# Kernel optimization log

Hardware: AMD Instinct MI355X
Metric: run time of the kernel (lower is better)

The kernel has to match this reference:

```python
import jax, jax.numpy as jnp
import numpy as np

B, T, IN, OUT = 32, 128, 512, 512
N, Wd, R, H = 128, 64, 4, 512      # memory slots, word size, read heads, controller size
EPS = 1e-6
IFACE = R * Wd + R + Wd + 1 + Wd + Wd + R + 1 + 1 + 3 * R  # DNC interface vector size


def setup_inputs() -> dict:
    key = jax.random.key(0)
    ks = jax.random.split(key, 6)
    s = jnp.float32(0.05)
    lstm_in = IN + R * Wd
    return {
        "input_sequence": jax.random.normal(ks[0], (B, T, IN), jnp.float32),
        "Wx": jax.random.normal(ks[1], (lstm_in, 4 * H), jnp.float32) * s,
        "Wh": jax.random.normal(ks[2], (H, 4 * H), jnp.float32) * s,
        "b_lstm": jnp.zeros((4 * H,), jnp.float32),
        "W_iface": jax.random.normal(ks[3], (H, IFACE), jnp.float32) * s,
        "b_iface": jnp.zeros((IFACE,), jnp.float32),
        "W_out": jax.random.normal(ks[4], (R * Wd + H, OUT), jnp.float32) * s,
        "b_out": jnp.zeros((OUT,), jnp.float32),
    }


def _alloc(u):
    """DNC allocation weighting for one example. u: [N] usage in [0,1]."""
    phi = jnp.argsort(u)                      # ascending usage (data-dependent gather)
    su = u[phi]
    cp = jnp.cumprod(su)
    cp_excl = jnp.concatenate([jnp.ones((1,), su.dtype), cp[:-1]])
    a_sorted = (1.0 - su) * cp_excl
    return jnp.zeros_like(u).at[phi].set(a_sorted)  # scatter back to original order


def _content(M, keys, beta):
    """Cosine content addressing. M: [B,N,W], keys: [B,K,W], beta: [B,K] -> [B,K,N]."""
    Mn = M / (jnp.linalg.norm(M, axis=-1, keepdims=True) + EPS)
    kn = keys / (jnp.linalg.norm(keys, axis=-1, keepdims=True) + EPS)
    sim = jnp.einsum('bnw,bkw->bkn', Mn, kn)
    return jax.nn.softmax(beta[..., None] * sim, axis=-1)


def _dnc_forward(input_sequence, Wx, Wh, b_lstm, W_iface, b_iface, W_out, b_out):
    eye = 1.0 - jnp.eye(N, dtype=jnp.float32)

    def step(carry, x_t):
        h, c, M, usage, link, prec, ww, wr, reads = carry
        # --- LSTM controller ---
        z = jnp.concatenate([x_t, reads], -1) @ Wx + h @ Wh + b_lstm
        i_g, f_g, g_g, o_g = jnp.split(z, 4, axis=-1)
        c_n = jax.nn.sigmoid(f_g) * c + jax.nn.sigmoid(i_g) * jnp.tanh(g_g)
        h_n = jax.nn.sigmoid(o_g) * jnp.tanh(c_n)
        # --- interface vector ---
        v = h_n @ W_iface + b_iface
        o = [0]
        def take(n):
            out = v[:, o[0]:o[0] + n]; o[0] += n; return out
        read_keys = take(R * Wd).reshape(B, R, Wd)
        read_beta = 1.0 + jax.nn.softplus(take(R))
        write_key = take(Wd).reshape(B, 1, Wd)
        write_beta = 1.0 + jax.nn.softplus(take(1))
        erase = jax.nn.sigmoid(take(Wd))
        write_vec = take(Wd)
        free = jax.nn.sigmoid(take(R))
        alloc_g = jax.nn.sigmoid(take(1))
        write_g = jax.nn.sigmoid(take(1))
        modes = jax.nn.softmax(take(3 * R).reshape(B, R, 3), axis=-1)
        # --- usage & allocation ---
        retention = jnp.prod(1.0 - free[:, :, None] * wr, axis=1)          # [B,N]
        usage_n = (usage + ww - usage * ww) * retention
        a = jax.vmap(_alloc)(usage_n)
        # --- write ---
        cw = _content(M, write_key, write_beta)[:, 0, :]                    # [B,N]
        ww_n = write_g * (alloc_g * a + (1.0 - alloc_g) * cw)
        M_n = M * (1.0 - ww_n[:, :, None] * erase[:, None, :]) + ww_n[:, :, None] * write_vec[:, None, :]
        # --- temporal link ---
        link_n = ((1.0 - ww_n[:, :, None] - ww_n[:, None, :]) * link
                  + ww_n[:, :, None] * prec[:, None, :]) * eye
        prec_n = (1.0 - ww_n.sum(-1, keepdims=True)) * prec + ww_n
        # --- read ---
        fw = jnp.einsum('bij,brj->bri', link_n, wr)
        bw = jnp.einsum('bji,brj->bri', link_n, wr)
        cr = _content(M_n, read_keys, read_beta)
        wr_n = modes[:, :, 0:1] * bw + modes[:, :, 1:2] * cr + modes[:, :, 2:3] * fw
        reads_n = jnp.einsum('brn,bnw->brw', wr_n, M_n).reshape(B, R * Wd)
        # --- output projection ---
        out = jnp.concatenate([reads_n, h_n], -1) @ W_out + b_out
        return (h_n, c_n, M_n, usage_n, link_n, prec_n, ww_n, wr_n, reads_n), out

    f32 = jnp.float32
    init = (jnp.zeros((B, H), f32), jnp.zeros((B, H), f32),
            jnp.zeros((B, N, Wd), f32), jnp.zeros((B, N), f32),
            jnp.zeros((B, N, N), f32), jnp.zeros((B, N), f32),
            jnp.zeros((B, N), f32), jnp.zeros((B, R, N), f32),
            jnp.zeros((B, R * Wd), f32))
    _, outs = jax.lax.scan(step, init, jnp.swapaxes(input_sequence, 0, 1))
    return jnp.swapaxes(outs, 0, 1)  # [B, T, OUT]


def reference(input_sequence, Wx, Wh, b_lstm, W_iface, b_iface, W_out, b_out):
    return _dnc_forward(input_sequence, Wx, Wh, b_lstm, W_iface, b_iface, W_out, b_out)
```

## Files before the change

### kernel.cpp

```cpp
#include <hip/hip_runtime.h>
#include <math.h>

#define TT 128
#define ZD 2048
#define IFC 471
#define EPSF 1e-6f
#define MST 66
#define LST 130
#define NBLK 256
#define UHT 24640
#define VHT 15424

#define FSP 16
#define NFLAGS 8192

#define D4(a,b) ((a).x*(b).x + (a).y*(b).y + (a).z*(b).z + (a).w*(b).w)

__device__ __forceinline__ float sig_(float x){ return 1.f/(1.f+expf(-x)); }
__device__ __forceinline__ float sp_(float x){ return fmaxf(x,0.f)+log1pf(expf(-fabsf(x))); }

__device__ __forceinline__ void st1(float* p, float v){
  unsigned u; __builtin_memcpy(&u,&v,4);
  __hip_atomic_store((unsigned*)p, u, __ATOMIC_RELAXED, __HIP_MEMORY_SCOPE_AGENT);
}
__device__ __forceinline__ void st2(float* p, float2 v){
  unsigned long long u; __builtin_memcpy(&u,&v,8);
  __hip_atomic_store((unsigned long long*)p, u, __ATOMIC_RELAXED, __HIP_MEMORY_SCOPE_AGENT);
}

__device__ __forceinline__ void arrive(unsigned* f, unsigned gen){
  __syncthreads();
  if (threadIdx.x == 0)
    __hip_atomic_store(f, gen, __ATOMIC_RELAXED, __HIP_MEMORY_SCOPE_AGENT);
}
__device__ __forceinline__ void wait_ge(const unsigned* f, int n, unsigned gen){
  if (threadIdx.x < 64){
    for (int i = threadIdx.x; i < n; i += 64){
      const unsigned* p = f + (size_t)i*FSP;
      if (__hip_atomic_load(p, __ATOMIC_RELAXED, __HIP_MEMORY_SCOPE_AGENT) >= gen) continue;
      int spins = 0; bool done = false;
      while (spins < 64){
        if (__hip_atomic_load(p, __ATOMIC_RELAXED, __HIP_MEMORY_SCOPE_AGENT) >= gen){ done = true; break; }
        __builtin_amdgcn_s_sleep(1); ++spins;
      }
      if (!done){
        while (__hip_atomic_load(p, __ATOMIC_RELAXED, __HIP_MEMORY_SCOPE_AGENT) < gen)
          __builtin_amdgcn_s_sleep(2);
      }
    }
  }
  __syncthreads();
}

__device__ __forceinline__ unsigned bf16rne(float f){
  unsigned u; __builtin_memcpy(&u,&f,4);
  return (u + 0x7fffu + ((u>>16)&1u)) >> 16;
}
__device__ __forceinline__ float bflo(unsigned w){
  unsigned u = w << 16; float f; __builtin_memcpy(&f,&u,4); return f;
}
__device__ __forceinline__ float bfhi(unsigned w){
  unsigned u = w & 0xffff0000u; float f; __builtin_memcpy(&f,&u,4); return f;
}

__global__ __launch_bounds__(256) void gemm_bias(
    const float* __restrict__ A, const float* __restrict__ B,
    const float* __restrict__ bias, float* __restrict__ C,
    int Nc, int K)
{
  __shared__ float As[16][68];
  __shared__ float Bs[16][68];
  const int tid = threadIdx.x;
  const int bx = blockIdx.x, by = blockIdx.y;
  const int tx = tid & 15, ty = tid >> 4;
  const int am = tid >> 2, ak = (tid & 3) * 4;
  const int bk = tid >> 4, bn = (tid & 15) * 4;
  float acc[4][4] = {};
  const float* Ap = A + (size_t)(by*64+am)*K + ak;
  const float* Bp = B + (size_t)bk*Nc + bx*64 + bn;
  for (int k0 = 0; k0 < K; k0 += 16) {
    float4 av = *(const float4*)Ap; Ap += 16;
    float4 bv = *(const float4*)Bp; Bp += (size_t)16*Nc;
    As[ak+0][am]=av.x; As[ak+1][am]=av.y; As[ak+2][am]=av.z; As[ak+3][am]=av.w;
    *(float4*)&Bs[bk][bn] = bv;
    __syncthreads();
#pragma unroll
    for (int kk = 0; kk < 16; ++kk) {
      float4 a4 = *(const float4*)&As[kk][ty*4];
      float4 b4 = *(const float4*)&Bs[kk][tx*4];
      acc[0][0]+=a4.x*b4.x; acc[0][1]+=a4.x*b4.y; acc[0][2]+=a4.x*b4.z; acc[0][3]+=a4.x*b4.w;
      acc[1][0]+=a4.y*b4.x; acc[1][1]+=a4.y*b4.y; acc[1][2]+=a4.y*b4.z; acc[1][3]+=a4.y*b4.w;
      acc[2][0]+=a4.z*b4.x; acc[2][1]+=a4.z*b4.y; acc[2][2]+=a4.z*b4.z; acc[2][3]+=a4.z*b4.w;
      acc[3][0]+=a4.w*b4.x; acc[3][1]+=a4.w*b4.y; acc[3][2]+=a4.w*b4.z; acc[3][3]+=a4.w*b4.w;
    }
    __syncthreads();
  }
  float4 bb = *(const float4*)(bias + bx*64 + tx*4);
#pragma unroll
  for (int i = 0; i < 4; ++i) {
    float4 o;
    o.x = acc[i][0]+bb.x; o.y = acc[i][1]+bb.y; o.z = acc[i][2]+bb.z; o.w = acc[i][3]+bb.w;
    *(float4*)(C + (size_t)(by*64+ty*4+i)*Nc + bx*64 + tx*4) = o;
  }
}

__global__ __launch_bounds__(256) void gemm_out(
    const float* __restrict__ A, const float* __restrict__ B,
    const float* __restrict__ bias, float* __restrict__ C)
{
  __shared__ float As[16][68];
  __shared__ float Bs[16][68];
  const int tid = threadIdx.x;
  const int bx = blockIdx.x, by = blockIdx.y;
  const int tx = tid & 15, ty = tid >> 4;
  const int am = tid >> 2, ak = (tid & 3) * 4;
  const int bk = tid >> 4, bn = (tid & 15) * 4;
  float acc[4][4] = {};
  const int arow = by*64 + am;
  const float* Ap = A + (size_t)(arow >> 5)*UHT + (size_t)(arow & 31)*768 + ak;
  const float* Bp = B + (size_t)bk*512 + bx*64 + bn;
  for (int k0 = 0; k0 < 768; k0 += 16) {
    float4 av = *(const float4*)Ap; Ap += 16;
    float4 bv = *(const float4*)Bp; Bp += (size_t)16*512;
    As[ak+0][am]=av.x; As[ak+1][am]=av.y; As[ak+2][am]=av.z; As[ak+3][am]=av.w;
    *(float4*)&Bs[bk][bn] = bv;
    __syncthreads();
#pragma unroll
    for (int kk = 0; kk < 16; ++kk) {
      float4 a4 = *(const float4*)&As[kk][ty*4];
      float4 b4 = *(const float4*)&Bs[kk][tx*4];
      acc[0][0]+=a4.x*b4.x; acc[0][1]+=a4.x*b4.y; acc[0][2]+=a4.x*b4.z; acc[0][3]+=a4.x*b4.w;
      acc[1][0]+=a4.y*b4.x; acc[1][1]+=a4.y*b4.y; acc[1][2]+=a4.y*b4.z; acc[1][3]+=a4.y*b4.w;
      acc[2][0]+=a4.z*b4.x; acc[2][1]+=a4.z*b4.y; acc[2][2]+=a4.z*b4.z; acc[2][3]+=a4.z*b4.w;
      acc[3][0]+=a4.w*b4.x; acc[3][1]+=a4.w*b4.y; acc[3][2]+=a4.w*b4.z; acc[3][3]+=a4.w*b4.w;
    }
    __syncthreads();
  }
  float4 bb = *(const float4*)(bias + bx*64 + tx*4);
#pragma unroll
  for (int i = 0; i < 4; ++i) {
    int row = by*64 + ty*4 + i;
    int crow = (row & 31)*128 + (row >> 5);
    float4 o;
    o.x = acc[i][0]+bb.x; o.y = acc[i][1]+bb.y; o.z = acc[i][2]+bb.z; o.w = acc[i][3]+bb.w;
    *(float4*)(C + (size_t)crow*512 + bx*64 + tx*4) = o;
  }
}

#define SL_L    0
#define SL_M    16640
#define SL_V    25088
#define SL_WR   25568
#define SL_FW   26080
#define SL_BW   26592
#define SL_CR   27104
#define SL_USG  27616
#define SL_PRC  27744
#define SL_WW   27872
#define SL_SU   28000
#define SL_CPX  28128
#define SL_MN   28256
#define SL_SW   28384
#define SL_CW   28512
#define SL_RNK  28640
#define SL_MSC  28768
#define SL_ER   28832
#define SL_WV   28896
#define SL_TOT  28960

#define CWI_U  29640
#define CUS_F  34096
#define CZH_F  37184
#define CCS_F  37488
#define CTOT_F 37564

__global__ void init_flags(unsigned* flags) {
  int idx = blockIdx.x*1024 + threadIdx.x;
  if (idx < NFLAGS)
    __hip_atomic_store(&flags[idx], 0u, __ATOMIC_RELAXED, __HIP_MEMORY_SCOPE_AGENT);
}

__global__ __launch_bounds__(1024) void dnc_coop(
    const float* __restrict__ Xproj, const float* __restrict__ Wx,
    const float* __restrict__ Wh, const float* __restrict__ Wif,
    const float* __restrict__ bif,
    float* __restrict__ Uh, float* __restrict__ Vh,
    unsigned* __restrict__ flags)
{
  const int blk = blockIdx.x, tid = threadIdx.x;
  extern __shared__ float sm[];
  const int g = blk & 7;
  const int role = blk >> 3;
  unsigned* FHg = flags + (size_t)g*64*FSP;
  unsigned* FVg = FHg + 28*FSP;
  unsigned* FRg = FHg + 56*FSP;

  if (role < 4) {
    const int eg = g*4 + role;
    float* L   = sm + SL_L;   float* Ms  = sm + SL_M;
    float* v   = sm + SL_V;   float* wr  = sm + SL_WR;
    float* fw  = sm + SL_FW;  float* bw  = sm + SL_BW;
    float* cr  = sm + SL_CR;  float* usg = sm + SL_USG;
    float* prc = sm + SL_PRC; float* ww  = sm + SL_WW;
    float* su  = sm + SL_SU;  float* cpx = sm + SL_CPX;
    float* Mn  = sm + SL_MN;  float* swv = sm + SL_SW;
    float* cw  = sm + SL_CW;  int*   rnk = (int*)(sm + SL_RNK);
    float* msc = sm + SL_MSC; float* er_ = sm + SL_ER; float* wv_ = sm + SL_WV;

    for (int i = tid; i < SL_TOT; i += 1024) sm[i] = 0.f;
    __syncthreads();

    for (int t = 0; t < TT; ++t) {
      wait_ge(FVg, 28, t+1);
      if (tid < IFC) v[tid] = Vh[(size_t)t*VHT + eg*480 + tid];
      __syncthreads();
      if (tid < 128) {
        float ret = 1.f;
#pragma unroll
        for (int r = 0; r < 4; ++r) { float fr = sig_(v[453+r]); ret *= 1.f - fr*wr[r*128+tid]; }
        float u = usg[tid], w_ = ww[tid];
        usg[tid] = (u + w_ - u*w_) * ret;
      } else if (tid < 256) {
        int n = tid - 128; float nk = 0.f, dot = 0.f;
#pragma unroll
        for (int w = 0; w < 64; w += 2) {
          float2 k2 = *(float2*)&v[260+w];
          float2 m2 = *(float2*)&Ms[n*MST+w];
          nk += k2.x*k2.x + k2.y*k2.y; dot += m2.x*k2.x + m2.y*k2.y;
        }
        float beta = 1.f + sp_(v[324]);
        swv[n] = beta * dot / ((Mn[n]+EPSF)*(sqrtf(nk)+EPSF));
      } else if (tid < 260) {
        int r = tid - 256; float s = 0.f;
#pragma unroll
        for (int w = 0; w < 64; w += 4) { float4 k4 = *(float4*)&v[r*64+w]; s += D4(k4,k4); }
        msc[1+r] = sqrtf(s);
      } else if (tid == 260) {
        for (int r = 0; r < 4; ++r) {
          float a0 = v[459+r*3], a1 = v[459+r*3+1], a2 = v[459+r*3+2];
          float mx = fmaxf(a0, fmaxf(a1, a2));
          float e0 = expf(a0-mx), e1 = expf(a1-mx), e2 = expf(a2-mx);
          float dn = e0+e1+e2;
          msc[8+r*3] = e0/dn; msc[8+r*3+1] = e1/dn; msc[8+r*3+2] = e2/dn;
        }
      } else if (tid >= 640 && tid < 704) { int w = tid-640; er_[w] = sig_(v[325+w]); }
      else if (tid >= 704 && tid < 768) { int w = tid-704; wv_[w] = v[389+w]; }
      __syncthreads();
      if (tid < 128) {
        float ui = usg[tid]; int rk = 0;
#pragma unroll
        for (int j = 0; j < 128; j += 4) {
          float4 u4 = *(float4*)&usg[j];
          rk += (u4.x < ui || (u4.x == ui && (j+0) < tid)) ? 1 : 0;
          rk += (u4.y < ui || (u4.y == ui && (j+1) < tid)) ? 1 : 0;
          rk += (u4.z < ui || (u4.z == ui && (j+2) < tid)) ? 1 : 0;
          rk += (u4.w < ui || (u4.w == ui && (j+3) < tid)) ? 1 : 0;
        }
        rnk[tid] = rk; su[rk] = ui;
      } else if (tid < 192) {
        int l = tid - 128;
        float s1 = swv[l], s2 = swv[l+64];
        float m = fmaxf(s1, s2);
#pragma unroll
        for (int o = 32; o > 0; o >>= 1) m = fmaxf(m, __shfl_xor(m, o));
        float e1 = expf(s1-m), e2 = expf(s2-m);
        float dn = e1 + e2;
#pragma unroll
        for (int o = 32; o > 0; o >>= 1) dn += __shfl_xor(dn, o);
        cw[l] = e1/dn; cw[l+64] = e2/dn;
      }
      __syncthreads();
      if (tid < 64) {
        float a0 = su[2*tid], a1 = su[2*tid+1];
        float p = a0*a1, sc = p;
#pragma unroll
        for (int off = 1; off < 64; off <<= 1) {
          float o = __shfl_up(sc, off);
          if ((int)tid >= off) sc *= o;
        }
        float ex = __shfl_up(sc, 1);
        if (tid == 0) ex = 1.f;
        cpx[2*tid] = ex;
        cpx[2*tid+1] = ex*a0;
        float ag = sig_(v[457]), wg = sig_(v[458]);
        float wwa[2];
#pragma unroll
        for (int q = 0; q < 2; ++q) {
          int n = 2*tid + q;
          float a_i = (1.f - usg[n]) * cpx[rnk[n]];
          wwa[q] = wg * (ag*a_i + (1.f-ag)*cw[n]);
          ww[n] = wwa[q];
        }
        float s = wwa[0] + wwa[1];
#pragma unroll
        for (int o = 32; o > 0; o >>= 1) s += __shfl_xor(s, o);
        if (tid == 0) msc[0] = s;
      }
      __syncthreads();
      {
        int n = tid >> 3, q = tid & 7;
        float wwn = ww[n];
        int w8 = q*8;
        float sq = 0.f;
#pragma unroll
        for (int gq = 0; gq < 4; ++gq) {
          int w = w8 + gq*2;
          float2 m = *(float2*)&Ms[n*MST+w];
          float2 e2 = *(float2*)&er_[w];
          float2 v2 = *(float2*)&wv_[w];
          m.x = m.x*(1.f - wwn*e2.x) + wwn*v2.x;
          m.y = m.y*(1.f - wwn*e2.y) + wwn*v2.y;
          *(float2*)&Ms[n*MST+w] = m;
          sq += m.x*m.x + m.y*m.y;
        }
        sq += __shfl_xor(sq,1); sq += __shfl_xor(sq,2); sq += __shfl_xor(sq,4);
        if (q == 0) Mn[n] = sqrtf(sq);
        int j16 = q*16;
#pragma unroll
        for (int gq = 0; gq < 8; ++gq) {
          int j = j16 + gq*2;
          float2 lv = *(float2*)&L[n*LST + j];
          float2 p2 = *(float2*)&prc[j];
          float2 w2 = *(float2*)&ww[j];
          lv.x = (1.f - wwn - w2.x)*lv.x + wwn*p2.x;
          lv.y = (1.f - wwn - w2.y)*lv.y + wwn*p2.y;
          int d = n - j;
          if (d == 0) lv.x = 0.f;
          if (d == 1) lv.y = 0.f;
          *(float2*)&L[n*LST + j] = lv;
        }
      }
      __syncthreads();
      if (tid < 256) {
        int half = tid >> 7, t2 = tid & 127;
        int i0 = (t2 >> 2) * 4, sg = t2 & 3;
        float4 av[4] = {{0,0,0,0},{0,0,0,0},{0,0,0,0},{0,0,0,0}};
        if (half == 0) {
#pragma unroll
          for (int m = 0; m < 8; ++m) {
            int j = sg*4 + m*16;
            float4 w0 = *(float4*)&wr[0*128+j];
            float4 w1 = *(float4*)&wr[1*128+j];
            float4 w2 = *(float4*)&wr[2*128+j];
            float4 w3 = *(float4*)&wr[3*128+j];
#pragma unroll
            for (int k = 0; k < 4; ++k) {
              float2 la = *(float2*)&L[(i0+k)*LST+j];
              float2 lb = *(float2*)&L[(i0+k)*LST+j+2];
              float dv0 = la.x*w0.x + la.y*w0.y + lb.x*w0.z + lb.y*w0.w;
              float dv1 = la.x*w1.x + la.y*w1.y + lb.x*w1.z + lb.y*w1.w;
              float dv2 = la.x*w2.x + la.y*w2.y + lb.x*w2.z + lb.y*w2.w;
              float dv3 = la.x*w3.x + la.y*w3.y + lb.x*w3.z + lb.y*w3.w;
              if (k == 0){ av[0].x+=dv0; av[1].x+=dv1; av[2].x+=dv2; av[3].x+=dv3; }
              if (k == 1){ av[0].y+=dv0; av[1].y+=dv1; av[2].y+=dv2; av[3].y+=dv3; }
              if (k == 2){ av[0].z+=dv0; av[1].z+=dv1; av[2].z+=dv2; av[3].z+=dv3; }
              if (k == 3){ av[0].w+=dv0; av[1].w+=dv1; av[2].w+=dv2; av[3].w+=dv3; }
            }
          }
        } else {
#pragma unroll
          for (int m = 0; m < 32; ++m) {
            int j = sg + m*4;
            float2 la = *(float2*)&L[j*LST + i0];
            float2 lb = *(float2*)&L[j*LST + i0 + 2];
            float w0 = wr[j], w1 = wr[128+j], w2 = wr[256+j], w3 = wr[384+j];
            av[0].x+=w0*la.x; av[0].y+=w0*la.y; av[0].z+=w0*lb.x; av[0].w+=w0*lb.y;
            av[1].x+=w1*la.x; av[1].y+=w1*la.y; av[1].z+=w1*lb.x; av[1].w+=w1*lb.y;
            av[2].x+=w2*la.x; av[2].y+=w2*la.y; av[2].z+=w2*lb.x; av[2].w+=w2*lb.y;
            av[3].x+=w3*la.x; av[3].y+=w3*la.y; av[3].z+=w3*lb.x; av[3].w+=w3*lb.y;
          }
        }
#pragma unroll
        for (int r = 0; r < 4; ++r) {
          av[r].x += __shfl_xor(av[r].x,1); av[r].x += __shfl_xor(av[r].x,2);
          av[r].y += __shfl_xor(av[r].y,1); av[r].y += __shfl_xor(av[r].y,2);
          av[r].z += __shfl_xor(av[r].z,1); av[r].z += __shfl_xor(av[r].z,2);
          av[r].w += __shfl_xor(av[r].w,1); av[r].w += __shfl_xor(av[r].w,2);
        }
        if (sg == 0) {
          float* dst = half ? bw : fw;
#pragma unroll
          for (int r = 0; r < 4; ++r) {
            dst[r*128 + i0+0] = av[r].x; dst[r*128 + i0+1] = av[r].y;
            dst[r*128 + i0+2] = av[r].z; dst[r*128 + i0+3] = av[r].w;
          }
        }
      } else if (tid < 384) {
        int n = tid - 256;
        prc[n] = (1.f - msc[0])*prc[n] + ww[n];
      } else if (tid >= 512) {
        int r = (tid >> 7) & 3, n = tid & 127;
        float dot = 0.f;
#pragma unroll
        for (int w = 0; w < 64; w += 2) {
          float2 m2 = *(float2*)&Ms[n*MST+w];
          float2 k2 = *(float2*)&v[r*64+w];
          dot += m2.x*k2.x + m2.y*k2.y;
        }
        float beta = 1.f + sp_(v[256+r]);
        cr[r*128+n] = beta * dot / ((Mn[n]+EPSF)*(msc[1+r]+EPSF));
      }
      __syncthreads();
      if (tid < 256) {
        int r = tid >> 6, l = tid & 63;
        float s1 = cr[r*128+l], s2 = cr[r*128+l+64];
        float m = fmaxf(s1, s2);
#pragma unroll
        for (int o = 32; o > 0; o >>= 1) m = fmaxf(m, __shfl_xor(m, o));
        float e1 = expf(s1-m), e2 = expf(s2-m);
        float dn = e1 + e2;
#pragma unroll
        for (int o = 32; o > 0; o >>= 1) dn += __shfl_xor(dn, o);
        float m0 = msc[8+r*3], m1 = msc[8+r*3+1], m2 = msc[8+r*3+2];
        wr[r*128+l]    = m0*bw[r*128+l]    + m1*(e1/dn) + m2*fw[r*128+l];
        wr[r*128+l+64] = m0*bw[r*128+l+64] + m1*(e2/dn) + m2*fw[r*128+l+64];
      }
      __syncthreads();
      if (tid < 512) {
        int r = tid >> 7, t2 = tid & 127;
        int w0 = (t2 >> 3) * 4, ns = t2 & 7;
        float4 a = {0,0,0,0};
#pragma unroll
        for (int m = 0; m < 16; ++m) {
          int n = ns + m*8;
          float2 ma = *(float2*)&Ms[n*MST + w0];
          float2 mb = *(float2*)&Ms[n*MST + w0 + 2];
          float wv = wr[r*128 + n];
          a.x += wv*ma.x; a.y += wv*ma.y; a.z += wv*mb.x; a.w += wv*mb.y;
        }
        a.x += __shfl_xor(a.x,1); a.x += __shfl_xor(a.x,2); a.x += __shfl_xor(a.x,4);
        a.y += __shfl_xor(a.y,1); a.y += __shfl_xor(a.y,2); a.y += __shfl_xor(a.y,4);
        a.z += __shfl_xor(a.z,1); a.z += __shfl_xor(a.z,2); a.z += __shfl_xor(a.z,4);
        a.w += __shfl_xor(a.w,1); a.w += __shfl_xor(a.w,2); a.w += __shfl_xor(a.w,4);
        if (ns == 0) {
          int o = r*64 + w0;
          float2 lo = {a.x, a.y}, hi = {a.z, a.w};
          st2(&Uh[(size_t)t*UHT + eg*768 + o], lo);
          st2(&Uh[(size_t)t*UHT + eg*768 + o + 2], hi);
        }
      }
      arrive(&FRg[role*FSP], t+1);
    }
  } else {
    const int c = role - 4;
    const int egB = g*4;
    const int d0 = (512*c)/28, d1 = (512*(c+1))/28, Dd = d1-d0, NJ = 4*Dd;
    const int v0 = (471*c)/28, v1 = (471*(c+1))/28, JV = v1-v0;
    unsigned* Wzu = (unsigned*)sm;
    unsigned* Wiu = (unsigned*)sm + CWI_U;
    float* us  = sm + CUS_F;
    float* zh  = sm + CZH_F;
    float* cst = sm + CCS_F;

    for (int idx = tid; idx < NJ*384; idx += 1024) {
      int j = idx/384, p = idx - j*384, k = 2*p;
      int q = j/Dd, di = j - q*Dd, gc = q*512 + d0 + di;
      float w0 = (k < 256) ? Wx[(size_t)(512+k)*ZD + gc] : Wh[(size_t)(k-256)*ZD + gc];
      float w1 = (k+1 < 256) ? Wx[(size_t)(513+k)*ZD + gc] : Wh[(size_t)(k-255)*ZD + gc];
      Wzu[j*390 + p] = bf16rne(w0) | (bf16rne(w1) << 16);
    }
    for (int idx = tid; idx < JV*256; idx += 1024) {
      int j = idx/256, p = idx - j*256, k = 2*p, gc = v0 + j;
      float w0 = Wif[(size_t)k*IFC + gc];
      float w1 = Wif[(size_t)(k+1)*IFC + gc];
      Wiu[j*262 + p] = bf16rne(w0) | (bf16rne(w1) << 16);
    }
    if (tid < 76) cst[tid] = 0.f;
    if (tid < 4*NJ) {
      int e = tid/NJ, j = tid - e*NJ;
      int q = j/Dd, di = j - q*Dd, gc = q*512 + d0 + di;
      zh[e*76 + j] = Xproj[((size_t)(egB+e)*TT + 0)*ZD + gc];
    }
    __syncthreads();
    if (tid < 4*Dd) {
      int e = tid/Dd, di = tid - e*Dd;
      float zi = zh[e*76 + di], zg = zh[e*76 + 2*Dd + di], zo = zh[e*76 + 3*Dd + di];
      float cn = sig_(zi)*tanhf(zg);
      float hn = sig_(zo)*tanhf(cn);
      cst[tid] = cn;
      st1(&Uh[(size_t)0*UHT + (egB + e)*768 + 256 + d0 + di], hn);
    }
    arrive(&FHg[c*FSP], 1);

    for (int t = 0; t < TT; ++t) {
      float xpre = 0.f; int pe = 0, pj = 0;
      if (t+1 < TT && tid < 4*NJ) {
        pe = tid/NJ; pj = tid - pe*NJ;
        int q = pj/Dd, di = pj - q*Dd, gc = q*512 + d0 + di;
        xpre = Xproj[((size_t)(egB+pe)*TT + t+1)*ZD + gc];
      }
      wait_ge(FHg, 28, t+1);
      if (tid < 512) {
        int e = tid >> 7, f4 = (tid & 127) * 4;
        *(float4*)&us[e*772 + 256 + f4] =
            *(const float4*)&Uh[(size_t)t*UHT + (egB+e)*768 + 256 + f4];
      }
      if (t+1 < TT && tid < 4*NJ) {
        zh[pe*76 + pj] = xpre;
      }
      __syncthreads();
      if (tid < 544) {
        int g8 = tid >> 3, ks = tid & 7;
        int e = g8/17, j = g8 - e*17;
        if (j < JV) {
          float acc = 0.f;
#pragma unroll 4
          for (int m = 0; m < 16; ++m) {
            int p = m*16 + ks*2;
            float4 hv = *(const float4*)&us[e*772 + 256 + 2*p];
            uint2 wu = *(const uint2*)&Wiu[j*262 + p];
            acc += hv.x*bflo(wu.x) + hv.y*bfhi(wu.x)
                 + hv.z*bflo(wu.y) + hv.w*bfhi(wu.y);
          }
          acc += __shfl_xor(acc,1); acc += __shfl_xor(acc,2); acc += __shfl_xor(acc,4);
          if (ks == 0) {
            int col = v0 + j;
            st1(&Vh[(size_t)t*VHT + (egB+e)*480 + col], bif[col] + acc);
          }
        }
      }
      arrive(&FVg[c*FSP], t+1);
      if (t+1 < TT) {
        if (tid < 608) {
          int q2 = tid >> 1, ks = tid & 1;
          int e = q2/76, j = q2 - e*76;
          if (j < NJ) {
            float acc = 0.f;
#pragma unroll 4
            for (int m = 0; m < 64; ++m) {
              int p = 128 + m*4 + ks*2;
              float4 hv = *(const float4*)&us[e*772 + 2*p];
              uint2 wu = *(const uint2*)&Wzu[j*390 + p];
              acc += hv.x*bflo(wu.x) + hv.y*bfhi(wu.x)
                   + hv.z*bflo(wu.y) + hv.w*bfhi(wu.y);
            }
            acc += __shfl_xor(acc,1);
            if (ks == 0) zh[e*76 + j] += acc;
          }
        }
        wait_ge(FRg, 4, t+1);
        if (tid < 256) {
          int e = tid >> 6, f4 = (tid & 63) * 4;
          *(float4*)&us[e*772 + f4] =
              *(const float4*)&Uh[(size_t)t*UHT + (egB+e)*768 + f4];
        }
        __syncthreads();
        if (tid < 608) {
          int q2 = tid >> 1, ks = tid & 1;
          int e = q2/76, j = q2 - e*76;
          if (j < NJ) {
            float acc = 0.f;
#pragma unroll 4
            for (int m = 0; m < 32; ++m) {
              int p = m*4 + ks*2;
              float4 rv = *(const float4*)&us[e*772 + 2*p];
              uint2 wu = *(const uint2*)&Wzu[j*390 + p];
              acc += rv.x*bflo(wu.x) + rv.y*bfhi(wu.x)
                   + rv.z*bflo(wu.y) + rv.w*bfhi(wu.y);
            }
            acc += __shfl_xor(acc,1);
            if (ks == 0) zh[e*76 + j] += acc;
          }
        }
        __syncthreads();
        if (tid < 4*Dd) {
          int e = tid/Dd, di = tid - e*Dd;
          float zi = zh[e*76 + di],      zf = zh[e*76 + Dd + di];
          float zg = zh[e*76 + 2*Dd+di], zo = zh[e*76 + 3*Dd + di];
          float cn = sig_(zf)*cst[tid] + sig_(zi)*tanhf(zg);
          float hn = sig_(zo)*tanhf(cn);
          cst[tid] = cn;
          st1(&Uh[(size_t)(t+1)*UHT + (egB+e)*768 + 256 + d0 + di], hn);
        }
        arrive(&FHg[c*FSP], t+2);
      }
    }
  }
}

extern "C" void kernel_launch(void* const* d_in, const int* in_sizes, int n_in,
                              void* d_out, int out_size, void* d_ws, size_t ws_size,
                              hipStream_t stream) {
  const float* x   = (const float*)d_in[0];
  const float* Wx  = (const float*)d_in[1];
  const float* Wh  = (const float*)d_in[2];
  const float* bl  = (const float*)d_in[3];
  const float* Wif = (const float*)d_in[4];
  const float* bif = (const float*)d_in[5];
  const float* Wo  = (const float*)d_in[6];
  const float* bo  = (const float*)d_in[7];
  float* out = (float*)d_out;

  unsigned* fl = (unsigned*)d_ws;
  float* Xp = (float*)(fl + NFLAGS);
  float* Uh = Xp + (size_t)4096*2048;
  float* Vh = Uh + (size_t)TT*UHT;

  gemm_bias<<<dim3(2048/64, 4096/64), dim3(256), 0, stream>>>(x, Wx, bl, Xp, 2048, 512);

  init_flags<<<dim3(8), dim3(1024), 0, stream>>>(fl);

  const int smem_bytes = CTOT_F * 4;
  (void)hipFuncSetAttribute((const void*)dnc_coop, hipFuncAttributeMaxDynamicSharedMemorySize, smem_bytes);
  void* args[] = { (void*)&Xp, (void*)&Wx, (void*)&Wh, (void*)&Wif, (void*)&bif,
                   (void*)&Uh, (void*)&Vh, (void*)&fl };
  (void)hipLaunchCooperativeKernel((void*)dnc_coop, dim3(NBLK), dim3(1024), args,
                                   (unsigned int)smem_bytes, stream);

  gemm_out<<<dim3(512/64, 4096/64), dim3(256), 0, stream>>>(Uh, Wo, bo, out);
}
```

Measured before the change: 3.953 ms.

## Replace block-wide flag waits with per-thread waits on the producing block's flag

The collective wait_ge barrier, where one wavefront polls every producer flag and then the block syncs, is replaced by per-thread spin1 calls. Each thread polls only the flag of the producer block that wrote the slice it loads. The read-vector fetch is also moved onto otherwise idle threads (640-895), so its wait overlaps with the hidden-state gate GEMV instead of following it. This removes serialized polling and the extra barrier on the recurrent critical path. In exchange many more threads poll global flags at once, and memory ordering now relies on relaxed per-thread loads.

New measurement: 4.091 ms. 3.5% more time.

```diff
diff --git a/kernel.cpp b/kernel.cpp
--- a/kernel.cpp
+++ b/kernel.cpp
@@ -33,23 +33,15 @@
   if (threadIdx.x == 0)
     __hip_atomic_store(f, gen, __ATOMIC_RELAXED, __HIP_MEMORY_SCOPE_AGENT);
 }
-__device__ __forceinline__ void wait_ge(const unsigned* f, int n, unsigned gen){
-  if (threadIdx.x < 64){
-    for (int i = threadIdx.x; i < n; i += 64){
-      const unsigned* p = f + (size_t)i*FSP;
-      if (__hip_atomic_load(p, __ATOMIC_RELAXED, __HIP_MEMORY_SCOPE_AGENT) >= gen) continue;
-      int spins = 0; bool done = false;
-      while (spins < 64){
-        if (__hip_atomic_load(p, __ATOMIC_RELAXED, __HIP_MEMORY_SCOPE_AGENT) >= gen){ done = true; break; }
-        __builtin_amdgcn_s_sleep(1); ++spins;
-      }
-      if (!done){
-        while (__hip_atomic_load(p, __ATOMIC_RELAXED, __HIP_MEMORY_SCOPE_AGENT) < gen)
-          __builtin_amdgcn_s_sleep(2);
-      }
-    }
+__device__ __forceinline__ void spin1(const unsigned* p, unsigned gen){
+  if (__hip_atomic_load(p, __ATOMIC_RELAXED, __HIP_MEMORY_SCOPE_AGENT) >= gen) return;
+  int spins = 0;
+  while (spins < 64){
+    if (__hip_atomic_load(p, __ATOMIC_RELAXED, __HIP_MEMORY_SCOPE_AGENT) >= gen) return;
+    __builtin_amdgcn_s_sleep(1); ++spins;
   }
-  __syncthreads();
+  while (__hip_atomic_load(p, __ATOMIC_RELAXED, __HIP_MEMORY_SCOPE_AGENT) < gen)
+    __builtin_amdgcn_s_sleep(2);
 }
 
 __device__ __forceinline__ unsigned bf16rne(float f){
@@ -207,12 +199,16 @@
     float* cw  = sm + SL_CW;  int*   rnk = (int*)(sm + SL_RNK);
     float* msc = sm + SL_MSC; float* er_ = sm + SL_ER; float* wv_ = sm + SL_WV;
 
+    const int vown = (tid < IFC) ? (28*tid + 27)/471 : 0;
+
     for (int i = tid; i < SL_TOT; i += 1024) sm[i] = 0.f;
     __syncthreads();
 
     for (int t = 0; t < TT; ++t) {
-      wait_ge(FVg, 28, t+1);
-      if (tid < IFC) v[tid] = Vh[(size_t)t*VHT + eg*480 + tid];
+      if (tid < IFC) {
+        spin1(&FVg[vown*FSP], t+1);
+        v[tid] = Vh[(size_t)t*VHT + eg*480 + tid];
+      }
       __syncthreads();
       if (tid < 128) {
         float ret = 1.f;
@@ -452,6 +448,10 @@
     float* zh  = sm + CZH_F;
     float* cst = sm + CCS_F;
 
+    const int hf4 = (tid & 127) * 4;
+    const int hc0 = (28*hf4 + 27) >> 9;
+    const int hc1 = (28*(hf4+3) + 27) >> 9;
+
     for (int idx = tid; idx < NJ*384; idx += 1024) {
       int j = idx/384, p = idx - j*384, k = 2*p;
       int q = j/Dd, di = j - q*Dd, gc = q*512 + d0 + di;
@@ -489,11 +489,12 @@
         int q = pj/Dd, di = pj - q*Dd, gc = q*512 + d0 + di;
         xpre = Xproj[((size_t)(egB+pe)*TT + t+1)*ZD + gc];
       }
-      wait_ge(FHg, 28, t+1);
       if (tid < 512) {
-        int e = tid >> 7, f4 = (tid & 127) * 4;
-        *(float4*)&us[e*772 + 256 + f4] =
-            *(const float4*)&Uh[(size_t)t*UHT + (egB+e)*768 + 256 + f4];
+        int e = tid >> 7;
+        spin1(&FHg[hc0*FSP], t+1);
+        if (hc1 != hc0) spin1(&FHg[hc1*FSP], t+1);
+        *(float4*)&us[e*772 + 256 + hf4] =
+            *(const float4*)&Uh[(size_t)t*UHT + (egB+e)*768 + 256 + hf4];
       }
       if (t+1 < TT && tid < 4*NJ) {
         zh[pe*76 + pj] = xpre;
@@ -537,12 +538,11 @@
             acc += __shfl_xor(acc,1);
             if (ks == 0) zh[e*76 + j] += acc;
           }
-        }
-        wait_ge(FRg, 4, t+1);
-        if (tid < 256) {
-          int e = tid >> 6, f4 = (tid & 63) * 4;
-          *(float4*)&us[e*772 + f4] =
-              *(const float4*)&Uh[(size_t)t*UHT + (egB+e)*768 + f4];
+        } else if (tid >= 640 && tid < 896) {
+          int e2 = (tid - 640) >> 6, f4b = ((tid - 640) & 63) * 4;
+          spin1(&FRg[e2*FSP], t+1);
+          *(float4*)&us[e2*772 + f4b] =
+              *(const float4*)&Uh[(size_t)t*UHT + (egB+e2)*768 + f4b];
         }
         __syncthreads();
         if (tid < 608) {
```
